# Kernel optimization log

Hardware: AMD Instinct MI355X
Metric: run time of the kernel (lower is better)

The kernel has to match this reference:

```python
import jax, jax.numpy as jnp
import numpy as np

B, H, W, D = 4, 64, 64, 256
NH = 8
HD = D // NH        # 32
R = 2               # reduction_ratio
SCALE = 1.0 / np.sqrt(HD).astype(np.float32)
EPS = 1e-5


def _layernorm(x, g, b):
    m = jnp.mean(x, axis=-1, keepdims=True)
    v = jnp.mean((x - m) ** 2, axis=-1, keepdims=True)
    return (x - m) * jax.lax.rsqrt(v + EPS) * g + b


def setup_inputs() -> dict:
    key = jax.random.key(0)
    ks = jax.random.split(key, 8)
    s = 0.02
    return {
        "x": jax.random.normal(ks[0], (B, H, W, D), jnp.float32),
        "de": jax.random.normal(ks[1], (B, H, W, D), jnp.float32),  # unused by module
        "ln1_g": jnp.ones((D,), jnp.float32),
        "ln1_b": jnp.zeros((D,), jnp.float32),
        "Wq": jax.random.normal(ks[2], (D, D), jnp.float32) * s,
        "bq": jnp.zeros((D,), jnp.float32),
        "Wk": jax.random.normal(ks[3], (D, D), jnp.float32) * s,
        "bk": jnp.zeros((D,), jnp.float32),
        "Wv": jax.random.normal(ks[4], (D, D), jnp.float32) * s,
        "bv": jnp.zeros((D,), jnp.float32),
        "Wmean": jax.random.normal(ks[5], (D, D), jnp.float32) * s,  # no bias
        "ln2_g": jnp.ones((D,), jnp.float32),
        "ln2_b": jnp.zeros((D,), jnp.float32),
        "Wo": jax.random.normal(ks[6], (D, D), jnp.float32) * s,
        "bo": jnp.zeros((D,), jnp.float32),
    }


def reference(x, de, ln1_g, ln1_b, Wq, bq, Wk, bk, Wv, bv, Wmean, ln2_g, ln2_b, Wo, bo):
    b, h, w, d = x.shape
    identity = x
    x_norm = _layernorm(x, ln1_g, ln1_b)
    q = x_norm @ Wq + bq                                   # [b,h,w,d]
    # shift_size == 0 -> no roll. Block-mean pool K/V by factor R.
    x_red = jnp.mean(x.reshape(b, h // R, R, w // R, R, d), axis=(2, 4))  # [b,h/R,w/R,d]
    x_red = x_red @ Wmean
    x_red_norm = _layernorm(x_red, ln2_g, ln2_b)
    k = x_red_norm @ Wk + bk
    v = x_red_norm @ Wv + bv
    # split heads: [b, NH, N, HD]
    qf = q.reshape(b, h * w, NH, HD).transpose(0, 2, 1, 3)
    kf = k.reshape(b, (h // R) * (w // R), NH, HD).transpose(0, 2, 1, 3)
    vf = v.reshape(b, (h // R) * (w // R), NH, HD).transpose(0, 2, 1, 3)
    attn = jax.nn.softmax(jnp.einsum('bhqd,bhkd->bhqk', qf, kf) * SCALE, axis=-1)
    out = jnp.einsum('bhqk,bhkd->bhqd', attn, vf)          # [b,NH,N,HD]
    out = out.transpose(0, 2, 1, 3).reshape(b, h, w, d)
    out = out @ Wo + bo
    out = out + identity
    return out, attn
```

## Files before the change

### kernel.cpp

```cpp
#include <hip/hip_runtime.h>

typedef __bf16 bf16x8 __attribute__((ext_vector_type(8)));
typedef __bf16 bf16x4 __attribute__((ext_vector_type(4)));
typedef float f32x4 __attribute__((ext_vector_type(4)));

#define SCALE 0.17677669529663687f

template<int MODE>
__device__ __forceinline__ void gemm_body(const __bf16* __restrict__ A,
    const __bf16* __restrict__ Wt, const float* __restrict__ bias,
    void* __restrict__ Cout, int bx, int by, int tid) {
  const int w = tid >> 6, l = tid & 63;
  const int col = l & 15, quad = l >> 4;
  const int row0 = bx * 64 + w * 16;
  const int col0 = by * 64;
  f32x4 acc[4] = {{0.f,0.f,0.f,0.f},{0.f,0.f,0.f,0.f},{0.f,0.f,0.f,0.f},{0.f,0.f,0.f,0.f}};
  const __bf16* ap = A + (size_t)(row0 + col) * 256 + quad * 8;
  #pragma unroll
  for (int ks = 0; ks < 8; ++ks) {
    bf16x8 af = *(const bf16x8*)(ap + ks * 32);
    #pragma unroll
    for (int n = 0; n < 4; ++n) {
      bf16x8 bf = *(const bf16x8*)(Wt + (size_t)(col0 + n * 16 + col) * 256 + ks * 32 + quad * 8);
      acc[n] = __builtin_amdgcn_mfma_f32_16x16x32_bf16(af, bf, acc[n], 0, 0, 0);
    }
  }
  const int rbase = row0 + quad * 4;
  #pragma unroll
  for (int n = 0; n < 4; ++n) {
    const int cc = col0 + n * 16 + col;
    const float bv = bias ? bias[cc] : 0.0f;
    if (MODE == 0) {
      __bf16* C = (__bf16*)Cout;
      #pragma unroll
      for (int r = 0; r < 4; ++r)
        C[(size_t)(rbase + r) * 256 + cc] = (__bf16)(acc[n][r] + bv);
    } else {
      __bf16* C = (__bf16*)Cout;
      const int bb2 = rbase >> 10, tl = rbase & 1023;
      bf16x4 o4;
      #pragma unroll
      for (int r = 0; r < 4; ++r) o4[r] = (__bf16)(acc[n][r] + bv);
      *(bf16x4*)(C + ((size_t)(bb2 * 256 + cc)) * 1024 + tl) = o4;
    }
  }
}

__global__ __launch_bounds__(256) void prep_kernel(
    const float* __restrict__ W0, const float* __restrict__ W1,
    const float* __restrict__ W2, const float* __restrict__ W3,
    const float* __restrict__ W4,
    __bf16* __restrict__ T0, __bf16* __restrict__ T1,
    __bf16* __restrict__ T2, __bf16* __restrict__ T3,
    __bf16* __restrict__ T4,
    const float* __restrict__ x, const float* __restrict__ g1,
    const float* __restrict__ b1, __bf16* __restrict__ xn,
    __bf16* __restrict__ xp) {
  const int blk = blockIdx.x, tid = threadIdx.x;
  if (blk < 1280) {
    int which = blk >> 8;
    const float* W = which == 0 ? W0 : which == 1 ? W1 : which == 2 ? W2 : which == 3 ? W3 : W4;
    __bf16* T = which == 0 ? T0 : which == 1 ? T1 : which == 2 ? T2 : which == 3 ? T3 : T4;
    int id = (blk & 255) * 256 + tid;
    int kk = id >> 8, n = id & 255;
    T[n * 256 + kk] = (__bf16)W[id];
  } else if (blk < 5376) {
    int wid = ((blk - 1280) * 256 + tid) >> 6;
    int lane = tid & 63;
    const float4 v = *(const float4*)(x + (size_t)wid * 256 + lane * 4);
    float s = v.x + v.y + v.z + v.w;
    #pragma unroll
    for (int off = 32; off; off >>= 1) s += __shfl_down(s, off);
    float mean = __shfl(s, 0) * (1.0f / 256.0f);
    float dx = v.x - mean, dy = v.y - mean, dz = v.z - mean, dw = v.w - mean;
    float vs = dx * dx + dy * dy + dz * dz + dw * dw;
    #pragma unroll
    for (int off = 32; off; off >>= 1) vs += __shfl_down(vs, off);
    float rstd = rsqrtf(__shfl(vs, 0) * (1.0f / 256.0f) + 1e-5f);
    const float4 gg = *(const float4*)(g1 + lane * 4);
    const float4 bv = *(const float4*)(b1 + lane * 4);
    bf16x4 o4;
    o4[0] = (__bf16)(dx * rstd * gg.x + bv.x);
    o4[1] = (__bf16)(dy * rstd * gg.y + bv.y);
    o4[2] = (__bf16)(dz * rstd * gg.z + bv.z);
    o4[3] = (__bf16)(dw * rstd * gg.w + bv.w);
    *(bf16x4*)(xn + (size_t)wid * 256 + lane * 4) = o4;
  } else {
    int idx = (blk - 5376) * 256 + tid;
    int t = idx >> 6, c4 = (idx & 63) << 2;
    int b = t >> 10, rem = t & 1023;
    int i = rem >> 5, j = rem & 31;
    size_t base = ((size_t)b * 4096 + i * 128 + j * 2) * 256 + c4;
    float4 a0 = *(const float4*)(x + base);
    float4 a1 = *(const float4*)(x + base + 256);
    float4 a2 = *(const float4*)(x + base + 16384);
    float4 a3 = *(const float4*)(x + base + 16640);
    bf16x4 o4;
    o4[0] = (__bf16)(0.25f * (a0.x + a1.x + a2.x + a3.x));
    o4[1] = (__bf16)(0.25f * (a0.y + a1.y + a2.y + a3.y));
    o4[2] = (__bf16)(0.25f * (a0.z + a1.z + a2.z + a3.z));
    o4[3] = (__bf16)(0.25f * (a0.w + a1.w + a2.w + a3.w));
    *(bf16x4*)(xp + (size_t)t * 256 + c4) = o4;
  }
}

__global__ __launch_bounds__(256) void qm_kernel(
    const __bf16* __restrict__ xn, const __bf16* __restrict__ WtQ,
    const float* __restrict__ bq, __bf16* __restrict__ qb,
    const __bf16* __restrict__ xp, const __bf16* __restrict__ WtM,
    const float* __restrict__ g2, const float* __restrict__ b2,
    __bf16* __restrict__ xr) {
  const int blk = blockIdx.x, tid = threadIdx.x;
  if (blk < 1024) {
    gemm_body<0>(xn, WtQ, bq, qb, blk & 255, blk >> 8, tid);
    return;
  }
  const int w = tid >> 6, l = tid & 63;
  const int col = l & 15, quad = l >> 4;
  const int row0 = (blk - 1024) * 64 + w * 16;
  f32x4 acc[16];
  #pragma unroll
  for (int n = 0; n < 16; ++n) acc[n] = (f32x4){0.f, 0.f, 0.f, 0.f};
  const __bf16* ap = xp + (size_t)(row0 + col) * 256 + quad * 8;
  #pragma unroll
  for (int ks = 0; ks < 8; ++ks) {
    bf16x8 af = *(const bf16x8*)(ap + ks * 32);
    #pragma unroll
    for (int n = 0; n < 16; ++n) {
      bf16x8 bf = *(const bf16x8*)(WtM + (size_t)(n * 16 + col) * 256 + ks * 32 + quad * 8);
      acc[n] = __builtin_amdgcn_mfma_f32_16x16x32_bf16(af, bf, acc[n], 0, 0, 0);
    }
  }
  #pragma unroll
  for (int r = 0; r < 4; ++r) {
    float s = 0.f;
    #pragma unroll
    for (int n = 0; n < 16; ++n) s += acc[n][r];
    #pragma unroll
    for (int m = 1; m < 16; m <<= 1) s += __shfl_xor(s, m);
    float mean = s * (1.0f / 256.0f);
    float vs = 0.f;
    #pragma unroll
    for (int n = 0; n < 16; ++n) { float d = acc[n][r] - mean; vs += d * d; }
    #pragma unroll
    for (int m = 1; m < 16; m <<= 1) vs += __shfl_xor(vs, m);
    float rstd = rsqrtf(vs * (1.0f / 256.0f) + 1e-5f);
    int row = row0 + quad * 4 + r;
    #pragma unroll
    for (int n = 0; n < 16; ++n) {
      int cc = n * 16 + col;
      xr[(size_t)row * 256 + cc] = (__bf16)((acc[n][r] - mean) * rstd * g2[cc] + b2[cc]);
    }
  }
}

__global__ __launch_bounds__(256) void kv_kernel(
    const __bf16* __restrict__ xr, const __bf16* __restrict__ WtK,
    const float* __restrict__ bk, __bf16* __restrict__ kbuf,
    const __bf16* __restrict__ WtV, const float* __restrict__ bv,
    __bf16* __restrict__ vTb) {
  const int blk = blockIdx.x, tid = threadIdx.x;
  if (blk < 256) gemm_body<0>(xr, WtK, bk, kbuf, blk & 63, blk >> 6, tid);
  else { int k = blk - 256; gemm_body<1>(xr, WtV, bv, vTb, k & 63, k >> 6, tid); }
}

__global__ __launch_bounds__(256) void o_kernel(
    const __bf16* __restrict__ oat, const __bf16* __restrict__ WtO,
    const float* __restrict__ bo, const float* __restrict__ resid,
    float* __restrict__ out) {
  __shared__ float sm[4][16][68];
  const int tid = threadIdx.x;
  const int w = tid >> 6, l = tid & 63;
  const int col = l & 15, quad = l >> 4;
  const int row0 = blockIdx.x * 64 + w * 16;
  const int col0 = blockIdx.y * 64;
  f32x4 acc[4] = {{0.f,0.f,0.f,0.f},{0.f,0.f,0.f,0.f},{0.f,0.f,0.f,0.f},{0.f,0.f,0.f,0.f}};
  const __bf16* ap = oat + (size_t)(row0 + col) * 256 + quad * 8;
  #pragma unroll
  for (int ks = 0; ks < 8; ++ks) {
    bf16x8 af = *(const bf16x8*)(ap + ks * 32);
    #pragma unroll
    for (int n = 0; n < 4; ++n) {
      bf16x8 bf = *(const bf16x8*)(WtO + (size_t)(col0 + n * 16 + col) * 256 + ks * 32 + quad * 8);
      acc[n] = __builtin_amdgcn_mfma_f32_16x16x32_bf16(af, bf, acc[n], 0, 0, 0);
    }
  }
  #pragma unroll
  for (int n = 0; n < 4; ++n) {
    const float bv = bo[col0 + n * 16 + col];
    #pragma unroll
    for (int r = 0; r < 4; ++r)
      sm[w][quad * 4 + r][n * 16 + col] = acc[n][r] + bv;
  }
  #pragma unroll
  for (int i = 0; i < 4; ++i) {
    int lr = i * 4 + quad;
    int f4 = l & 15;
    size_t off = (size_t)(row0 + lr) * 256 + col0 + f4 * 4;
    float4 rv = *(const float4*)(resid + off);
    const float* sp = &sm[w][lr][f4 * 4];
    float4 ov;
    ov.x = sp[0] + rv.x; ov.y = sp[1] + rv.y;
    ov.z = sp[2] + rv.z; ov.w = sp[3] + rv.w;
    *(float4*)(out + off) = ov;
  }
}

__device__ __forceinline__ int swz(int row, int c) {
  return row * 1024 + (c ^ ((row & 7) << 2));
}

__global__ __launch_bounds__(256) void attn_fused(
    const __bf16* __restrict__ q, const __bf16* __restrict__ kb,
    const __bf16* __restrict__ vT, float* __restrict__ attn,
    __bf16* __restrict__ oat) {
  __shared__ float Ss[16 * 1024];
  __shared__ float part[64 * 32];
  const int tid = threadIdx.x;
  const int w = tid >> 6, l = tid & 63;
  const int col = l & 15, quad = l >> 4;
  const int bh = blockIdx.y, b = bh >> 3, h = bh & 7;
  const __bf16* kbase = kb + ((size_t)(b * 1024 + col)) * 256 + h * 32 + quad * 8;
  const __bf16* v0p = vT + ((size_t)(b * 256 + h * 32 + col)) * 1024;
  const __bf16* v1p = v0p + 16 * 1024;

  for (int tile = 0; tile < 2; ++tile) {
    const int q0 = blockIdx.x * 32 + tile * 16;

    bf16x8 qf = *(const bf16x8*)(q + ((size_t)(b * 4096 + q0 + col)) * 256 + h * 32 + quad * 8);
    #pragma unroll 4
    for (int t = 0; t < 16; ++t) {
      int j0 = w * 256 + t * 16;
      bf16x8 kf = *(const bf16x8*)(kbase + (size_t)j0 * 256);
      f32x4 c = {0.f, 0.f, 0.f, 0.f};
      c = __builtin_amdgcn_mfma_f32_16x16x32_bf16(qf, kf, c, 0, 0, 0);
      #pragma unroll
      for (int r = 0; r < 4; ++r)
        Ss[swz(quad * 4 + r, j0 + col)] = c[r] * SCALE;
    }
    __syncthreads();

    float* abase = attn + ((size_t)bh * 4096 + q0) * 1024;
    #pragma unroll
    for (int rr = 0; rr < 4; ++rr) {
      int row = w * 4 + rr;
      f32x4 v4[4];
      float m = -1e30f;
      #pragma unroll
      for (int i = 0; i < 4; ++i) {
        v4[i] = *(const f32x4*)(&Ss[swz(row, i * 256 + l * 4)]);
        m = fmaxf(m, fmaxf(fmaxf(v4[i][0], v4[i][1]), fmaxf(v4[i][2], v4[i][3])));
      }
      #pragma unroll
      for (int off = 32; off; off >>= 1) m = fmaxf(m, __shfl_down(m, off));
      m = __shfl(m, 0);
      float s = 0.f;
      #pragma unroll
      for (int i = 0; i < 4; ++i) {
        v4[i][0] = __expf(v4[i][0] - m); v4[i][1] = __expf(v4[i][1] - m);
        v4[i][2] = __expf(v4[i][2] - m); v4[i][3] = __expf(v4[i][3] - m);
        s += v4[i][0] + v4[i][1] + v4[i][2] + v4[i][3];
      }
      #pragma unroll
      for (int off = 32; off; off >>= 1) s += __shfl_down(s, off);
      float inv = 1.0f / __shfl(s, 0);
      float* arow = abase + (size_t)row * 1024;
      #pragma unroll
      for (int i = 0; i < 4; ++i) {
        v4[i][0] *= inv; v4[i][1] *= inv; v4[i][2] *= inv; v4[i][3] *= inv;
        *(f32x4*)(&Ss[swz(row, i * 256 + l * 4)]) = v4[i];
        __builtin_nontemporal_store(v4[i], (f32x4*)(arow + i * 256 + l * 4));
      }
    }
    __syncthreads();

    f32x4 a0 = {0.f, 0.f, 0.f, 0.f}, a1 = {0.f, 0.f, 0.f, 0.f};
    #pragma unroll 2
    for (int s8 = 0; s8 < 8; ++s8) {
      int k0 = w * 256 + s8 * 32;
      int c0 = k0 + quad * 8;
      f32x4 p0 = *(const f32x4*)(&Ss[swz(col, c0)]);
      f32x4 p1 = *(const f32x4*)(&Ss[swz(col, c0 + 4)]);
      bf16x8 af;
      af[0] = (__bf16)p0[0]; af[1] = (__bf16)p0[1]; af[2] = (__bf16)p0[2]; af[3] = (__bf16)p0[3];
      af[4] = (__bf16)p1[0]; af[5] = (__bf16)p1[1]; af[6] = (__bf16)p1[2]; af[7] = (__bf16)p1[3];
      bf16x8 b0 = *(const bf16x8*)(v0p + k0 + quad * 8);
      bf16x8 b1 = *(const bf16x8*)(v1p + k0 + quad * 8);
      a0 = __builtin_amdgcn_mfma_f32_16x16x32_bf16(af, b0, a0, 0, 0, 0);
      a1 = __builtin_amdgcn_mfma_f32_16x16x32_bf16(af, b1, a1, 0, 0, 0);
    }

    #pragma unroll
    for (int r = 0; r < 4; ++r) {
      part[(w * 16 + quad * 4 + r) * 32 + col] = a0[r];
      part[(w * 16 + quad * 4 + r) * 32 + 16 + col] = a1[r];
    }
    __syncthreads();
    int idx = tid;
    #pragma unroll
    for (int it = 0; it < 2; ++it, idx += 256) {
      int row = idx >> 5, d = idx & 31;
      float sum = part[row * 32 + d] + part[(16 + row) * 32 + d]
                + part[(32 + row) * 32 + d] + part[(48 + row) * 32 + d];
      oat[((size_t)(b * 4096 + q0 + row)) * 256 + h * 32 + d] = (__bf16)sum;
    }
  }
}

extern "C" void kernel_launch(void* const* d_in, const int* in_sizes, int n_in,
                              void* d_out, int out_size, void* d_ws, size_t ws_size,
                              hipStream_t stream) {
  (void)in_sizes; (void)n_in; (void)out_size; (void)ws_size;
  const float* x     = (const float*)d_in[0];
  const float* ln1_g = (const float*)d_in[2];
  const float* ln1_b = (const float*)d_in[3];
  const float* Wq    = (const float*)d_in[4];
  const float* bq    = (const float*)d_in[5];
  const float* Wk    = (const float*)d_in[6];
  const float* bk    = (const float*)d_in[7];
  const float* Wv    = (const float*)d_in[8];
  const float* bv    = (const float*)d_in[9];
  const float* Wmean = (const float*)d_in[10];
  const float* ln2_g = (const float*)d_in[11];
  const float* ln2_b = (const float*)d_in[12];
  const float* Wo    = (const float*)d_in[13];
  const float* bo    = (const float*)d_in[14];

  float* out  = (float*)d_out;
  float* attn = out + 4194304;

  __bf16* w0   = (__bf16*)d_ws;
  __bf16* xn   = w0;
  __bf16* qb   = w0 + 4194304;
  __bf16* oat  = w0 + 8388608;
  __bf16* xp   = w0 + 12582912;
  __bf16* xr   = w0 + 14680064;
  __bf16* kbuf = w0 + 15728640;
  __bf16* vTb  = w0 + 16777216;
  __bf16* WtQ  = w0 + 17825792;
  __bf16* WtK  = WtQ + 65536;
  __bf16* WtV  = WtK + 65536;
  __bf16* WtM  = WtV + 65536;
  __bf16* WtO  = WtM + 65536;

  prep_kernel<<<6400, 256, 0, stream>>>(Wq, Wk, Wv, Wmean, Wo,
                                        WtQ, WtK, WtV, WtM, WtO,
                                        x, ln1_g, ln1_b, xn, xp);
  qm_kernel<<<1088, 256, 0, stream>>>(xn, WtQ, bq, qb, xp, WtM, ln2_g, ln2_b, xr);
  kv_kernel<<<512, 256, 0, stream>>>(xr, WtK, bk, kbuf, WtV, bv, vTb);
  attn_fused<<<dim3(128, 32), 256, 0, stream>>>(qb, kbuf, vTb, attn, oat);
  o_kernel<<<dim3(256, 4), 256, 0, stream>>>(oat, WtO, bo, x, out);
}
```

Baseline: 716.1 us.

## Keep attention scores in registers with split softmax and fuse pooling into layernorm

The attention kernel now keeps each wave's QK^T scores in registers. It computes a per-wave max and sum, then merges them across waves through a small shared stats array. This replaces the fp32 score tile in LDS and its row-wise softmax pass. P is written to LDS as swizzled bf16 so the PV MFMA reads it directly, and the kernel uses lighter barriers, MFMA priority hints and a 3-waves occupancy hint. The prep kernel fuses 2x2 pooling into the layernorm blocks by reusing the loaded x rows through LDS, which removes a second read of x. Register pressure from 16 f32x4 accumulators may limit occupancy.

Result: slower. 755.1 us (+5.4%).

```diff
diff --git a/kernel.cpp b/kernel.cpp
--- a/kernel.cpp
+++ b/kernel.cpp
@@ -56,6 +56,7 @@
     const float* __restrict__ x, const float* __restrict__ g1,
     const float* __restrict__ b1, __bf16* __restrict__ xn,
     __bf16* __restrict__ xp) {
+  __shared__ float4 plds[4][64];
   const int blk = blockIdx.x, tid = threadIdx.x;
   if (blk < 1280) {
     int which = blk >> 8;
@@ -64,43 +65,42 @@
     int id = (blk & 255) * 256 + tid;
     int kk = id >> 8, n = id & 255;
     T[n * 256 + kk] = (__bf16)W[id];
-  } else if (blk < 5376) {
-    int wid = ((blk - 1280) * 256 + tid) >> 6;
-    int lane = tid & 63;
-    const float4 v = *(const float4*)(x + (size_t)wid * 256 + lane * 4);
-    float s = v.x + v.y + v.z + v.w;
-    #pragma unroll
-    for (int off = 32; off; off >>= 1) s += __shfl_down(s, off);
-    float mean = __shfl(s, 0) * (1.0f / 256.0f);
-    float dx = v.x - mean, dy = v.y - mean, dz = v.z - mean, dw = v.w - mean;
-    float vs = dx * dx + dy * dy + dz * dz + dw * dw;
-    #pragma unroll
-    for (int off = 32; off; off >>= 1) vs += __shfl_down(vs, off);
-    float rstd = rsqrtf(__shfl(vs, 0) * (1.0f / 256.0f) + 1e-5f);
-    const float4 gg = *(const float4*)(g1 + lane * 4);
-    const float4 bv = *(const float4*)(b1 + lane * 4);
-    bf16x4 o4;
-    o4[0] = (__bf16)(dx * rstd * gg.x + bv.x);
-    o4[1] = (__bf16)(dy * rstd * gg.y + bv.y);
-    o4[2] = (__bf16)(dz * rstd * gg.z + bv.z);
-    o4[3] = (__bf16)(dw * rstd * gg.w + bv.w);
-    *(bf16x4*)(xn + (size_t)wid * 256 + lane * 4) = o4;
-  } else {
-    int idx = (blk - 5376) * 256 + tid;
-    int t = idx >> 6, c4 = (idx & 63) << 2;
-    int b = t >> 10, rem = t & 1023;
-    int i = rem >> 5, j = rem & 31;
-    size_t base = ((size_t)b * 4096 + i * 128 + j * 2) * 256 + c4;
-    float4 a0 = *(const float4*)(x + base);
-    float4 a1 = *(const float4*)(x + base + 256);
-    float4 a2 = *(const float4*)(x + base + 16384);
-    float4 a3 = *(const float4*)(x + base + 16640);
-    bf16x4 o4;
-    o4[0] = (__bf16)(0.25f * (a0.x + a1.x + a2.x + a3.x));
-    o4[1] = (__bf16)(0.25f * (a0.y + a1.y + a2.y + a3.y));
-    o4[2] = (__bf16)(0.25f * (a0.z + a1.z + a2.z + a3.z));
-    o4[3] = (__bf16)(0.25f * (a0.w + a1.w + a2.w + a3.w));
-    *(bf16x4*)(xp + (size_t)t * 256 + c4) = o4;
+    return;
+  }
+  const int w = tid >> 6, lane = tid & 63;
+  const int blk2 = blk - 1280;
+  const int b = blk2 >> 10, rem = blk2 & 1023;
+  const int qi = rem >> 5, qj = rem & 31;
+  const int i = qi * 2 + (w >> 1), j = qj * 2 + (w & 1);
+  const size_t tok = (size_t)b * 4096 + i * 64 + j;
+  const float4 v = *(const float4*)(x + tok * 256 + lane * 4);
+  plds[w][lane] = v;
+  float s = v.x + v.y + v.z + v.w;
+  #pragma unroll
+  for (int off = 32; off; off >>= 1) s += __shfl_down(s, off);
+  float mean = __shfl(s, 0) * (1.0f / 256.0f);
+  float dx = v.x - mean, dy = v.y - mean, dz = v.z - mean, dw = v.w - mean;
+  float vs = dx * dx + dy * dy + dz * dz + dw * dw;
+  #pragma unroll
+  for (int off = 32; off; off >>= 1) vs += __shfl_down(vs, off);
+  float rstd = rsqrtf(__shfl(vs, 0) * (1.0f / 256.0f) + 1e-5f);
+  const float4 gg = *(const float4*)(g1 + lane * 4);
+  const float4 bv = *(const float4*)(b1 + lane * 4);
+  bf16x4 o4;
+  o4[0] = (__bf16)(dx * rstd * gg.x + bv.x);
+  o4[1] = (__bf16)(dy * rstd * gg.y + bv.y);
+  o4[2] = (__bf16)(dz * rstd * gg.z + bv.z);
+  o4[3] = (__bf16)(dw * rstd * gg.w + bv.w);
+  *(bf16x4*)(xn + tok * 256 + lane * 4) = o4;
+  __syncthreads();
+  if (w == 0) {
+    float4 a0 = plds[0][lane], a1 = plds[1][lane], a2 = plds[2][lane], a3 = plds[3][lane];
+    bf16x4 p4;
+    p4[0] = (__bf16)(0.25f * (a0.x + a1.x + a2.x + a3.x));
+    p4[1] = (__bf16)(0.25f * (a0.y + a1.y + a2.y + a3.y));
+    p4[2] = (__bf16)(0.25f * (a0.z + a1.z + a2.z + a3.z));
+    p4[3] = (__bf16)(0.25f * (a0.w + a1.w + a2.w + a3.w));
+    *(bf16x4*)(xp + ((size_t)(b * 1024 + qi * 32 + qj)) * 256 + lane * 4) = p4;
   }
 }
 
@@ -206,20 +206,25 @@
   }
 }
 
-__device__ __forceinline__ int swz(int row, int c) {
-  return row * 1024 + (c ^ ((row & 7) << 2));
-}
-
-__global__ __launch_bounds__(256) void attn_fused(
+__device__ __forceinline__ void bar_nodrain() {
+  __builtin_amdgcn_sched_barrier(0);
+  asm volatile("s_waitcnt lgkmcnt(0)" ::: "memory");
+  __builtin_amdgcn_s_barrier();
+  __builtin_amdgcn_sched_barrier(0);
+}
+
+__global__ __launch_bounds__(256, 3) void attn_fused(
     const __bf16* __restrict__ q, const __bf16* __restrict__ kb,
     const __bf16* __restrict__ vT, float* __restrict__ attn,
     __bf16* __restrict__ oat) {
-  __shared__ float Ss[16 * 1024];
-  __shared__ float part[64 * 32];
+  __shared__ __bf16 Pb[16 * 1024];
+  __shared__ float2 stats[64];
+  float* Pf = (float*)Pb;
   const int tid = threadIdx.x;
   const int w = tid >> 6, l = tid & 63;
   const int col = l & 15, quad = l >> 4;
   const int bh = blockIdx.y, b = bh >> 3, h = bh & 7;
+  const int sw = (col & 7) << 3;
   const __bf16* kbase = kb + ((size_t)(b * 1024 + col)) * 256 + h * 32 + quad * 8;
   const __bf16* v0p = vT + ((size_t)(b * 256 + h * 32 + col)) * 1024;
   const __bf16* v1p = v0p + 16 * 1024;
@@ -228,81 +233,88 @@
     const int q0 = blockIdx.x * 32 + tile * 16;
 
     bf16x8 qf = *(const bf16x8*)(q + ((size_t)(b * 4096 + q0 + col)) * 256 + h * 32 + quad * 8);
-    #pragma unroll 4
+    f32x4 s[16];
+    __builtin_amdgcn_s_setprio(1);
+    #pragma unroll
     for (int t = 0; t < 16; ++t) {
-      int j0 = w * 256 + t * 16;
-      bf16x8 kf = *(const bf16x8*)(kbase + (size_t)j0 * 256);
-      f32x4 c = {0.f, 0.f, 0.f, 0.f};
-      c = __builtin_amdgcn_mfma_f32_16x16x32_bf16(qf, kf, c, 0, 0, 0);
-      #pragma unroll
-      for (int r = 0; r < 4; ++r)
-        Ss[swz(quad * 4 + r, j0 + col)] = c[r] * SCALE;
-    }
-    __syncthreads();
-
-    float* abase = attn + ((size_t)bh * 4096 + q0) * 1024;
-    #pragma unroll
-    for (int rr = 0; rr < 4; ++rr) {
-      int row = w * 4 + rr;
-      f32x4 v4[4];
-      float m = -1e30f;
-      #pragma unroll
-      for (int i = 0; i < 4; ++i) {
-        v4[i] = *(const f32x4*)(&Ss[swz(row, i * 256 + l * 4)]);
-        m = fmaxf(m, fmaxf(fmaxf(v4[i][0], v4[i][1]), fmaxf(v4[i][2], v4[i][3])));
-      }
-      #pragma unroll
-      for (int off = 32; off; off >>= 1) m = fmaxf(m, __shfl_down(m, off));
-      m = __shfl(m, 0);
-      float s = 0.f;
-      #pragma unroll
-      for (int i = 0; i < 4; ++i) {
-        v4[i][0] = __expf(v4[i][0] - m); v4[i][1] = __expf(v4[i][1] - m);
-        v4[i][2] = __expf(v4[i][2] - m); v4[i][3] = __expf(v4[i][3] - m);
-        s += v4[i][0] + v4[i][1] + v4[i][2] + v4[i][3];
-      }
-      #pragma unroll
-      for (int off = 32; off; off >>= 1) s += __shfl_down(s, off);
-      float inv = 1.0f / __shfl(s, 0);
-      float* arow = abase + (size_t)row * 1024;
-      #pragma unroll
-      for (int i = 0; i < 4; ++i) {
-        v4[i][0] *= inv; v4[i][1] *= inv; v4[i][2] *= inv; v4[i][3] *= inv;
-        *(f32x4*)(&Ss[swz(row, i * 256 + l * 4)]) = v4[i];
-        __builtin_nontemporal_store(v4[i], (f32x4*)(arow + i * 256 + l * 4));
-      }
-    }
-    __syncthreads();
+      bf16x8 kf = *(const bf16x8*)(kbase + (size_t)(w * 256 + t * 16) * 256);
+      s[t] = __builtin_amdgcn_mfma_f32_16x16x32_bf16(kf, qf,
+              (f32x4){0.f, 0.f, 0.f, 0.f}, 0, 0, 0);
+    }
+    __builtin_amdgcn_s_setprio(0);
+
+    f32x4 m4 = s[0];
+    #pragma unroll
+    for (int t = 1; t < 16; ++t) {
+      m4[0] = fmaxf(m4[0], s[t][0]); m4[1] = fmaxf(m4[1], s[t][1]);
+      m4[2] = fmaxf(m4[2], s[t][2]); m4[3] = fmaxf(m4[3], s[t][3]);
+    }
+    float m = fmaxf(fmaxf(m4[0], m4[1]), fmaxf(m4[2], m4[3])) * SCALE;
+    m = fmaxf(m, __shfl_xor(m, 16));
+    m = fmaxf(m, __shfl_xor(m, 32));
+    f32x4 s4 = {0.f, 0.f, 0.f, 0.f};
+    #pragma unroll
+    for (int t = 0; t < 16; ++t) {
+      s[t][0] = __expf(fmaf(s[t][0], SCALE, -m)); s4[0] += s[t][0];
+      s[t][1] = __expf(fmaf(s[t][1], SCALE, -m)); s4[1] += s[t][1];
+      s[t][2] = __expf(fmaf(s[t][2], SCALE, -m)); s4[2] += s[t][2];
+      s[t][3] = __expf(fmaf(s[t][3], SCALE, -m)); s4[3] += s[t][3];
+    }
+    float sum = (s4[0] + s4[1]) + (s4[2] + s4[3]);
+    sum += __shfl_xor(sum, 16);
+    sum += __shfl_xor(sum, 32);
+    if (l < 16) stats[w * 16 + col] = make_float2(m, sum);
+    bar_nodrain();
+
+    float2 e0 = stats[col], e1 = stats[16 + col], e2 = stats[32 + col], e3 = stats[48 + col];
+    float gm = fmaxf(fmaxf(e0.x, e1.x), fmaxf(e2.x, e3.x));
+    float gs = e0.y * __expf(e0.x - gm) + e1.y * __expf(e1.x - gm)
+             + e2.y * __expf(e2.x - gm) + e3.y * __expf(e3.x - gm);
+    float f = __expf(m - gm) / gs;
+
+    float* arow = attn + ((size_t)(bh * 4096 + q0 + col)) * 1024 + w * 256 + quad * 4;
+    __bf16* prow = Pb + col * 1024;
+    const int kb0 = w * 256 + quad * 4;
+    #pragma unroll
+    for (int t = 0; t < 16; ++t) {
+      f32x4 pv;
+      pv[0] = s[t][0] * f; pv[1] = s[t][1] * f;
+      pv[2] = s[t][2] * f; pv[3] = s[t][3] * f;
+      __builtin_nontemporal_store(pv, (f32x4*)(arow + t * 16));
+      bf16x4 pbv;
+      pbv[0] = (__bf16)pv[0]; pbv[1] = (__bf16)pv[1];
+      pbv[2] = (__bf16)pv[2]; pbv[3] = (__bf16)pv[3];
+      *(bf16x4*)(prow + (((kb0 + t * 16)) ^ sw)) = pbv;
+    }
+    bar_nodrain();
 
     f32x4 a0 = {0.f, 0.f, 0.f, 0.f}, a1 = {0.f, 0.f, 0.f, 0.f};
-    #pragma unroll 2
+    __builtin_amdgcn_s_setprio(1);
+    #pragma unroll
     for (int s8 = 0; s8 < 8; ++s8) {
-      int k0 = w * 256 + s8 * 32;
-      int c0 = k0 + quad * 8;
-      f32x4 p0 = *(const f32x4*)(&Ss[swz(col, c0)]);
-      f32x4 p1 = *(const f32x4*)(&Ss[swz(col, c0 + 4)]);
-      bf16x8 af;
-      af[0] = (__bf16)p0[0]; af[1] = (__bf16)p0[1]; af[2] = (__bf16)p0[2]; af[3] = (__bf16)p0[3];
-      af[4] = (__bf16)p1[0]; af[5] = (__bf16)p1[1]; af[6] = (__bf16)p1[2]; af[7] = (__bf16)p1[3];
-      bf16x8 b0 = *(const bf16x8*)(v0p + k0 + quad * 8);
-      bf16x8 b1 = *(const bf16x8*)(v1p + k0 + quad * 8);
+      int k0 = w * 256 + s8 * 32 + quad * 8;
+      bf16x8 af = *(const bf16x8*)(Pb + col * 1024 + (k0 ^ sw));
+      bf16x8 b0 = *(const bf16x8*)(v0p + k0);
+      bf16x8 b1 = *(const bf16x8*)(v1p + k0);
       a0 = __builtin_amdgcn_mfma_f32_16x16x32_bf16(af, b0, a0, 0, 0, 0);
       a1 = __builtin_amdgcn_mfma_f32_16x16x32_bf16(af, b1, a1, 0, 0, 0);
     }
+    __builtin_amdgcn_s_setprio(0);
 
     #pragma unroll
     for (int r = 0; r < 4; ++r) {
-      part[(w * 16 + quad * 4 + r) * 32 + col] = a0[r];
-      part[(w * 16 + quad * 4 + r) * 32 + 16 + col] = a1[r];
-    }
-    __syncthreads();
-    int idx = tid;
-    #pragma unroll
-    for (int it = 0; it < 2; ++it, idx += 256) {
+      Pf[(quad * 4 + r) * 512 + w * 128 + col] = a0[r];
+      Pf[(quad * 4 + r) * 512 + w * 128 + 16 + col] = a1[r];
+    }
+    bar_nodrain();
+
+    #pragma unroll
+    for (int it = 0; it < 2; ++it) {
+      int idx = tid + it * 256;
       int row = idx >> 5, d = idx & 31;
-      float sum = part[row * 32 + d] + part[(16 + row) * 32 + d]
-                + part[(32 + row) * 32 + d] + part[(48 + row) * 32 + d];
-      oat[((size_t)(b * 4096 + q0 + row)) * 256 + h * 32 + d] = (__bf16)sum;
+      float ssum = Pf[row * 512 + d] + Pf[row * 512 + 128 + d]
+                 + Pf[row * 512 + 256 + d] + Pf[row * 512 + 384 + d];
+      oat[((size_t)(b * 4096 + q0 + row)) * 256 + h * 32 + d] = (__bf16)ssum;
     }
   }
 }
@@ -343,7 +355,7 @@
   __bf16* WtM  = WtV + 65536;
   __bf16* WtO  = WtM + 65536;
 
-  prep_kernel<<<6400, 256, 0, stream>>>(Wq, Wk, Wv, Wmean, Wo,
+  prep_kernel<<<5376, 256, 0, stream>>>(Wq, Wk, Wv, Wmean, Wo,
                                         WtQ, WtK, WtV, WtM, WtO,
                                         x, ln1_g, ln1_b, xn, xp);
   qm_kernel<<<1088, 256, 0, stream>>>(xn, WtQ, bq, qb, xp, WtM, ln2_g, ln2_b, xr);
```
